# Kernel optimization log

Hardware: AMD Instinct MI355X
Metric: run time of the kernel (lower is better)

## Reference

```python
import jax, jax.numpy as jnp
import numpy as np

B, DIM, H, W = 2, 256, 64, 64
HEADS, DIM_HEAD = 8, 64
DIM_INNER = HEADS * DIM_HEAD  # 512


def setup_inputs() -> dict:
    key = jax.random.key(0)
    k1, k2, k3 = jax.random.split(key, 3)
    fmap = jax.random.normal(k1, (B, DIM, H, W), dtype=jnp.float32)
    # 1x1 convs == channel matmuls; store as [out_ch, in_ch]
    w_qkv = jax.random.normal(k2, (3 * DIM_INNER, DIM), dtype=jnp.float32) * (DIM ** -0.5)
    w_out = jax.random.normal(k3, (DIM, DIM_INNER), dtype=jnp.float32) * (DIM_INNER ** -0.5)
    return {"fmap": fmap, "w_qkv": w_qkv, "w_out": w_out}


def reference(fmap, w_qkv, w_out):
    b, c, x, y = fmap.shape
    n = x * y
    h, d = HEADS, DIM_HEAD
    xt = fmap.reshape(b, c, n)                       # [B, C, N]
    qkv = jnp.einsum('oc,bcn->bon', w_qkv, xt)        # [B, 3*h*d, N]
    q, k, v = jnp.split(qkv, 3, axis=1)               # each [B, h*d, N]
    # -> [B, h, N, d]
    to_bhnd = lambda t: t.reshape(b, h, d, n).transpose(0, 1, 3, 2)
    q, k, v = to_bhnd(q), to_bhnd(k), to_bhnd(v)
    # Euclidean distance matrix (torch.cdist p=2)
    q2 = jnp.sum(q * q, axis=-1)                      # [B, h, N]
    k2 = jnp.sum(k * k, axis=-1)                      # [B, h, N]
    qk = jnp.einsum('bhid,bhjd->bhij', q, k)          # [B, h, N, N]
    sim = jnp.sqrt(jnp.maximum(q2[..., :, None] + k2[..., None, :] - 2.0 * qk, 0.0))
    attn = jax.nn.softmax(sim, axis=-1)
    out = jnp.einsum('bhij,bhjd->bhid', attn, v)      # [B, h, N, d]
    out = out.transpose(0, 1, 3, 2).reshape(b, h * d, n)  # [B, h*d, N]
    out = jnp.einsum('oc,bcn->bon', w_out, out)       # [B, dim, N]
    return out.reshape(b, c, x, y)
```

## Files before the change

kernel.cpp:

```cpp
#include <hip/hip_runtime.h>

#define B_      2
#define DIM_    256
#define N_      4096
#define HEADS_  8
#define DINNER_ 512

typedef _Float16 half_t;
typedef _Float16 half8  __attribute__((ext_vector_type(8)));
typedef _Float16 half4v __attribute__((ext_vector_type(4)));
typedef _Float16 half2v __attribute__((ext_vector_type(2)));
typedef float    floatx4 __attribute__((ext_vector_type(4)));

#define SCL_    1.4426950408889634f
#define SHIFT2_ 20.0f


__global__ __launch_bounds__(256) void prep_all(const float* __restrict__ fmap,
                                                const float* __restrict__ w_qkv,
                                                const float* __restrict__ w_out,
                                                half_t* __restrict__ wqF,
                                                half_t* __restrict__ woF,
                                                half_t* __restrict__ xTg) {
    const int t = threadIdx.x, bx = blockIdx.x;
    __shared__ float Tl[64 * 68];
    if (bx < 96) {
        half_t* dst = wqF + (size_t)bx * 4096;
#pragma unroll
        for (int j = 0; j < 2; ++j) {
            const int cch = j * 256 + t;
            const int o = cch >> 4, m15 = cch & 15;
            const float4 a  = *(const float4*)&w_qkv[(size_t)(bx * 16 + m15) * 256 + o * 8];
            const float4 bb = *(const float4*)&w_qkv[(size_t)(bx * 16 + m15) * 256 + o * 8 + 4];
            half8 hv;
            hv[0] = (half_t)a.x;  hv[1] = (half_t)a.y;  hv[2] = (half_t)a.z;  hv[3] = (half_t)a.w;
            hv[4] = (half_t)bb.x; hv[5] = (half_t)bb.y; hv[6] = (half_t)bb.z; hv[7] = (half_t)bb.w;
            *(half8*)(dst + o * 128 + m15 * 8) = hv;
        }
    } else if (bx < 112) {
        const int mt = bx - 96;
        half_t* dst = woF + (size_t)mt * 8192;
#pragma unroll
        for (int j = 0; j < 4; ++j) {
            const int cch = j * 256 + t;
            const int o = cch >> 4, m15 = cch & 15;
            const float4 a  = *(const float4*)&w_out[(size_t)(mt * 16 + m15) * 512 + o * 8];
            const float4 bb = *(const float4*)&w_out[(size_t)(mt * 16 + m15) * 512 + o * 8 + 4];
            half8 hv;
            hv[0] = (half_t)a.x;  hv[1] = (half_t)a.y;  hv[2] = (half_t)a.z;  hv[3] = (half_t)a.w;
            hv[4] = (half_t)bb.x; hv[5] = (half_t)bb.y; hv[6] = (half_t)bb.z; hv[7] = (half_t)bb.w;
            *(half8*)(dst + o * 128 + m15 * 8) = hv;
        }
    } else {
        const int idx = bx - 112;
        const int n0 = (idx & 63) * 64, k0 = ((idx >> 6) & 3) * 64, b = idx >> 8;
        {
            const int kk = t >> 2, nq = (t & 3) * 16;
#pragma unroll
            for (int q = 0; q < 4; ++q) {
                float4 v = *(const float4*)&fmap[((size_t)b * DIM_ + k0 + kk) * N_ + n0 + nq + 4 * q];
                *(float4*)&Tl[kk * 68 + nq + 4 * q] = v;
            }
        }
        __syncthreads();
        {
            const int n = t >> 2, ko = (t & 3) * 16;
            half8 h0, h1;
#pragma unroll
            for (int j = 0; j < 8; ++j) h0[j] = (half_t)Tl[(ko + j) * 68 + n];
#pragma unroll
            for (int j = 0; j < 8; ++j) h1[j] = (half_t)Tl[(ko + 8 + j) * 68 + n];
            half_t* dst = xTg + (((size_t)b * 64 + (n0 >> 6)) * 4 + (k0 >> 6)) * 4096;
            const int o0 = ((ko >> 5) * 4 + (n >> 4)) * 512 + (((ko >> 3) & 3) * 16 + (n & 15)) * 8;
            const int k8 = ko + 8;
            const int o1 = ((k8 >> 5) * 4 + (n >> 4)) * 512 + (((k8 >> 3) & 3) * 16 + (n & 15)) * 8;
            *(half8*)(dst + o0) = h0;
            *(half8*)(dst + o1) = h1;
        }
    }
}

__global__ __launch_bounds__(256) void mm_qkv_mf(const half_t* __restrict__ wqF,
                                                 const half_t* __restrict__ xTg,
                                                 half_t* __restrict__ perm,
                                                 float* __restrict__ sq) {
    const int nt64 = blockIdx.x, by = blockIdx.y, b = blockIdx.z;
    const int t = threadIdx.x, w = t >> 6, L = t & 63, c = L & 15, g = L >> 4;
    const int mt = by * 4 + w;

    const half_t* Ab = wqF + (size_t)mt * 4096;
    const half_t* Bb = xTg + (((size_t)b * 64 + nt64) * 4) * 4096;

    __shared__ __align__(16) char smraw[8192 + 4352];
    half_t* VtH = (half_t*)smraw;
    float*  red = (float*)(smraw + 8192);

    const floatx4 fz = {0.f, 0.f, 0.f, 0.f};
    floatx4 acc[4];
#pragma unroll
    for (int ns = 0; ns < 4; ++ns) acc[ns] = fz;

#pragma unroll
    for (int kc = 0; kc < 8; ++kc) {
        const half8 af = *(const half8*)(Ab + (kc * 4 + g) * 128 + c * 8);
        const half_t* Bs = Bb + (kc >> 1) * 4096 + (kc & 1) * 2048;
#pragma unroll
        for (int ns = 0; ns < 4; ++ns) {
            const half8 bf = *(const half8*)(Bs + ns * 512 + L * 8);
            acc[ns] = __builtin_amdgcn_mfma_f32_16x16x32_f16(af, bf, acc[ns], 0, 0, 0);
        }
    }

    half_t* dst = perm + (((size_t)(b * 24 + by) * 64 + nt64) << 12);
    if (by < 16) {
        float part[4];
#pragma unroll
        for (int ns = 0; ns < 4; ++ns) {
            half_t hv[4];
            float s = 0.f;
#pragma unroll
            for (int i = 0; i < 4; ++i) {
                hv[i] = (half_t)(acc[ns][i] * SCL_);
                const float f = (float)hv[i];
                s = fmaf(f, f, s);
            }
            part[ns] = s;
            const int off = ((w >> 1) * 4 + ns) * 512 + (((2 * w + (g >> 1)) & 3) * 16 + c) * 8 + 4 * (g & 1);
            half2v p0, p1;
            p0[0] = hv[0]; p0[1] = hv[1];
            p1[0] = hv[2]; p1[1] = hv[3];
            *(half2v*)(VtH + off)     = p0;
            *(half2v*)(VtH + off + 2) = p1;
        }
#pragma unroll
        for (int ns = 0; ns < 4; ++ns)
            red[(ns * 16 + (w * 4 + g)) * 17 + c] = part[ns];
        __syncthreads();
#pragma unroll
        for (int j = 0; j < 2; ++j)
            *(half8*)(dst + t * 16 + j * 8) = *(half8*)(VtH + t * 16 + j * 8);
        if (t < 64) {
            const int ns = t >> 4, cc = t & 15;
            float s = 0.f;
#pragma unroll
            for (int wg = 0; wg < 16; ++wg) s += red[(ns * 16 + wg) * 17 + cc];
            const int tens = by >> 3, hh = by & 7;
            sq[((size_t)(tens * 16 + b * 8 + hh)) * N_ + nt64 * 64 + ns * 16 + cc] = s;
        }
    } else {
#pragma unroll
        for (int ns = 0; ns < 4; ++ns)
#pragma unroll
            for (int i = 0; i < 4; ++i)
                VtH[((ns >> 1) * 4 + w) * 512 + ((c >> 2) * 16 + 4 * g + i) * 8 + (ns & 1) * 4 + (c & 3)] =
                    (half_t)acc[ns][i];
        __syncthreads();
#pragma unroll
        for (int j = 0; j < 2; ++j)
            *(half8*)(dst + t * 16 + j * 8) = *(half8*)(VtH + t * 16 + j * 8);
    }
}

__global__ __launch_bounds__(512) void attn_mfma(const half_t* __restrict__ perm,
                                                 const float* __restrict__ sq,
                                                 half_t* __restrict__ oh,
                                                 float* __restrict__ lbuf) {
    const int bx = blockIdx.x;
    const int qb = bx & 15, kh = bx >> 4;
    const int h = blockIdx.y, b = blockIdx.z;
    const int bh = b * HEADS_ + h;

    const half_t* Qb = perm + ((size_t)(b * 24 + h) << 18);
    const half_t* Kb = perm + ((size_t)(b * 24 + 8 + h) << 18);
    const half_t* Vb = perm + ((size_t)(b * 24 + 16 + h) << 18);
    const float* q2a = sq + (size_t)bh * N_;
    const float* k2a = sq + (size_t)(16 + bh) * N_;

    __shared__ __align__(16) half_t Kl[2][4096];
    __shared__ __align__(16) half_t Vl[2][4096];
    __shared__ __align__(16) float  k2l[1024];

    const int t = threadIdx.x, w = t >> 6, L = t & 63, c = L & 15, g = L >> 4;
    const floatx4 fz = {0.f, 0.f, 0.f, 0.f};

    *(float2*)&k2l[t * 2] = *(const float2*)&k2a[kh * 1024 + t * 2];

    const int tl = w >> 1;
    const int p0 = (w & 1) * 2, p1 = p0 + 1;
    const half_t* Qt = Qb + ((size_t)(qb * 4 + tl) << 12);
    const half8 bq0a = *(const half8*)(Qt + (0 * 4 + p0) * 512 + L * 8);
    const half8 bq1a = *(const half8*)(Qt + (1 * 4 + p0) * 512 + L * 8);
    const half8 bq0b = *(const half8*)(Qt + (0 * 4 + p1) * 512 + L * 8);
    const half8 bq1b = *(const half8*)(Qt + (1 * 4 + p1) * 512 + L * 8);
    const float q2la = q2a[qb * 256 + 64 * tl + 16 * p0 + c];
    const float q2lb = q2a[qb * 256 + 64 * tl + 16 * p1 + c];

    half8 aone8;
    {
        const half_t ov = (c == 0) ? (half_t)1.0f : (half_t)0.0f;
        aone8[0] = ov; aone8[1] = ov; aone8[2] = ov; aone8[3] = ov;
        aone8[4] = ov; aone8[5] = ov; aone8[6] = ov; aone8[7] = ov;
    }

    floatx4 Oa[4], Ob[4];
    floatx4 laca = fz, lacb = fz;
#pragma unroll
    for (int dt = 0; dt < 4; ++dt) { Oa[dt] = fz; Ob[dt] = fz; }

    const int kt0 = kh * 16;
    half8 rk = *(const half8*)(Kb + ((size_t)kt0 << 12) + t * 8);
    half8 rv = *(const half8*)(Vb + ((size_t)kt0 << 12) + t * 8);

    union H8 { half8 v; half2v h2[4]; };

    for (int it = 0; it < 16; ++it) {
        const int buf = it & 1;
        *(half8*)(&Kl[buf][t * 8]) = rk;
        *(half8*)(&Vl[buf][t * 8]) = rv;
        asm volatile("s_waitcnt lgkmcnt(0)\n\ts_barrier" ::: "memory");
        if (it < 15) {
            rk = *(const half8*)(Kb + ((size_t)(kt0 + it + 1) << 12) + t * 8);
            rv = *(const half8*)(Vb + ((size_t)(kt0 + it + 1) << 12) + t * 8);
        }

#pragma unroll
        for (int ntp = 0; ntp < 2; ++ntp) {
            H8 ua, ub;
#pragma unroll
            for (int hh = 0; hh < 2; ++hh) {
                const int nt = ntp * 2 + hh;
                const half8 ak0 = *(const half8*)(&Kl[buf][(0 * 4 + nt) * 512 + L * 8]);
                const half8 ak1 = *(const half8*)(&Kl[buf][(1 * 4 + nt) * 512 + L * 8]);
                floatx4 Sa = __builtin_amdgcn_mfma_f32_16x16x32_f16(ak0, bq0a, fz, 0, 0, 0);
                Sa = __builtin_amdgcn_mfma_f32_16x16x32_f16(ak1, bq1a, Sa, 0, 0, 0);
                floatx4 Sb = __builtin_amdgcn_mfma_f32_16x16x32_f16(ak0, bq0b, fz, 0, 0, 0);
                Sb = __builtin_amdgcn_mfma_f32_16x16x32_f16(ak1, bq1b, Sb, 0, 0, 0);
                const float4 k2v = *(const float4*)&k2l[it * 64 + 16 * nt + 4 * g];

                float pa[4], pb[4];
                const float k2arr[4] = {k2v.x, k2v.y, k2v.z, k2v.w};
#pragma unroll
                for (int i = 0; i < 4; ++i) {
                    pa[i] = __builtin_amdgcn_exp2f(
                        __builtin_amdgcn_sqrtf(__builtin_fabsf(fmaf(Sa[i], -2.0f, q2la + k2arr[i]))) - SHIFT2_);
                    pb[i] = __builtin_amdgcn_exp2f(
                        __builtin_amdgcn_sqrtf(__builtin_fabsf(fmaf(Sb[i], -2.0f, q2lb + k2arr[i]))) - SHIFT2_);
                }
                ua.h2[2 * hh]     = __builtin_bit_cast(half2v, __builtin_amdgcn_cvt_pkrtz(pa[0], pa[1]));
                ua.h2[2 * hh + 1] = __builtin_bit_cast(half2v, __builtin_amdgcn_cvt_pkrtz(pa[2], pa[3]));
                ub.h2[2 * hh]     = __builtin_bit_cast(half2v, __builtin_amdgcn_cvt_pkrtz(pb[0], pb[1]));
                ub.h2[2 * hh + 1] = __builtin_bit_cast(half2v, __builtin_amdgcn_cvt_pkrtz(pb[2], pb[3]));
            }

            laca = __builtin_amdgcn_mfma_f32_16x16x32_f16(aone8, ua.v, laca, 0, 0, 0);
            lacb = __builtin_amdgcn_mfma_f32_16x16x32_f16(aone8, ub.v, lacb, 0, 0, 0);
#pragma unroll
            for (int dt = 0; dt < 4; ++dt) {
                const half8 av = *(const half8*)(&Vl[buf][(ntp * 4 + dt) * 512 + L * 8]);
                Oa[dt] = __builtin_amdgcn_mfma_f32_16x16x32_f16(av, ua.v, Oa[dt], 0, 0, 0);
                Ob[dt] = __builtin_amdgcn_mfma_f32_16x16x32_f16(av, ub.v, Ob[dt], 0, 0, 0);
            }
        }
    }

    const int ntile = qb * 4 + tl;
    half_t* dst = oh + (size_t)kh * 4194304 + (((size_t)bh * 64 + ntile) << 12);
#pragma unroll
    for (int dt = 0; dt < 4; ++dt) {
        const int obase = ((dt >> 1) * 4) * 512 + (((2 * dt + (g >> 1)) & 3) * 16 + c) * 8 + 4 * (g & 1);
        const half2v a0 = __builtin_bit_cast(half2v, __builtin_amdgcn_cvt_pkrtz(Oa[dt][0], Oa[dt][1]));
        const half2v a1 = __builtin_bit_cast(half2v, __builtin_amdgcn_cvt_pkrtz(Oa[dt][2], Oa[dt][3]));
        *(half2v*)(dst + obase + p0 * 512)     = a0;
        *(half2v*)(dst + obase + p0 * 512 + 2) = a1;
        const half2v b0 = __builtin_bit_cast(half2v, __builtin_amdgcn_cvt_pkrtz(Ob[dt][0], Ob[dt][1]));
        const half2v b1 = __builtin_bit_cast(half2v, __builtin_amdgcn_cvt_pkrtz(Ob[dt][2], Ob[dt][3]));
        *(half2v*)(dst + obase + p1 * 512)     = b0;
        *(half2v*)(dst + obase + p1 * 512 + 2) = b1;
    }
    if (L < 16) {
        const size_t lb0 = (size_t)kh * 65536 + (size_t)bh * N_ + qb * 256 + 64 * tl;
        lbuf[lb0 + 16 * p0 + L] = laca[0];
        lbuf[lb0 + 16 * p1 + L] = lacb[0];
    }
}

__global__ __launch_bounds__(256) void mm_out_mf(const half_t* __restrict__ woF,
                                                 const half_t* __restrict__ oh,
                                                 const float* __restrict__ lbuf,
                                                 float* __restrict__ out) {
    const int nt64 = blockIdx.x, mb = blockIdx.y, b = blockIdx.z;
    const int t = threadIdx.x, w = t >> 6, L = t & 63, c = L & 15, g = L >> 4;
    const int mt = mb * 4 + w;

    const half_t* Ab = woF + (size_t)mt * 8192;
    const floatx4 fz = {0.f, 0.f, 0.f, 0.f};
    floatx4 O4[4];
#pragma unroll
    for (int ns = 0; ns < 4; ++ns) O4[ns] = fz;

    __shared__ __align__(16) half_t sh[2][4096];
    __shared__ float lsh[2][64];

    half8 r0[4], r1[4];
    float lr[4];

    auto LOADH = [&](int h) {
        const size_t toff = (((size_t)(b * 8 + h) * 64 + nt64) << 12) + t * 16;
#pragma unroll
        for (int q = 0; q < 4; ++q) {
            r0[q] = *(const half8*)(oh + (size_t)q * 4194304 + toff);
            r1[q] = *(const half8*)(oh + (size_t)q * 4194304 + toff + 8);
        }
        if (t < 64) {
            const size_t li = (size_t)(b * 8 + h) * N_ + nt64 * 64 + t;
#pragma unroll
            for (int q = 0; q < 4; ++q) lr[q] = lbuf[(size_t)q * 65536 + li];
        }
    };

    LOADH(0);
    for (int h = 0; h < 8; ++h) {
        const int buf = h & 1;
        const half8 s0 = (r0[0] + r0[1]) + (r0[2] + r0[3]);
        const half8 s1 = (r1[0] + r1[1]) + (r1[2] + r1[3]);
        *(half8*)(&sh[buf][t * 16])     = s0;
        *(half8*)(&sh[buf][t * 16 + 8]) = s1;
        if (t < 64)
            lsh[buf][t] = __builtin_amdgcn_rcpf((lr[0] + lr[1]) + (lr[2] + lr[3]));
        __syncthreads();
        if (h < 7) LOADH(h + 1);

        floatx4 acc[4];
#pragma unroll
        for (int ns = 0; ns < 4; ++ns) acc[ns] = fz;
#pragma unroll
        for (int c2 = 0; c2 < 2; ++c2) {
            const half8 af = *(const half8*)(Ab + (h * 8 + c2 * 4 + g) * 128 + c * 8);
#pragma unroll
            for (int ns = 0; ns < 4; ++ns) {
                const half8 bf = *(const half8*)(&sh[buf][(c2 * 4 + ns) * 512 + L * 8]);
                acc[ns] = __builtin_amdgcn_mfma_f32_16x16x32_f16(af, bf, acc[ns], 0, 0, 0);
            }
        }
#pragma unroll
        for (int ns = 0; ns < 4; ++ns) {
            const float inv = lsh[buf][ns * 16 + c];
#pragma unroll
            for (int i = 0; i < 4; ++i) O4[ns][i] = fmaf(acc[ns][i], inv, O4[ns][i]);
        }
    }

    float* Cg = out + ((size_t)b * DIM_ + mt * 16) * N_ + nt64 * 64;
#pragma unroll
    for (int ns = 0; ns < 4; ++ns)
#pragma unroll
        for (int i = 0; i < 4; ++i)
            Cg[(size_t)(4 * g + i) * N_ + ns * 16 + c] = O4[ns][i];
}

extern "C" void kernel_launch(void* const* d_in, const int* in_sizes, int n_in,
                              void* d_out, int out_size, void* d_ws, size_t ws_size,
                              hipStream_t stream) {
    const float* fmap  = (const float*)d_in[0];
    const float* w_qkv = (const float*)d_in[1];
    const float* w_out = (const float*)d_in[2];
    float* out = (float*)d_out;

    char* ws = (char*)d_ws;
    half_t* perm = (half_t*)ws;
    float*  sq   = (float*) (ws + 25165824);
    float*  lbuf = (float*) (ws + 25690112);
    half_t* woF  = (half_t*)(ws + 26738688);
    half_t* oh   = (half_t*)(ws + 27000832);
    half_t* xTg  = (half_t*)(ws + 27000832);
    half_t* wqF  = (half_t*)(ws + 31195136);

    prep_all <<<624, 256, 0, stream>>>(fmap, w_qkv, w_out, wqF, woF, xTg);
    mm_qkv_mf<<<dim3(64, 24, 2), 256, 0, stream>>>(wqF, xTg, perm, sq);
    attn_mfma<<<dim3(64, 8, 2), 512, 0, stream>>>(perm, sq, oh, lbuf);
    mm_out_mf<<<dim3(64, 4, 2), 256, 0, stream>>>(woF, oh, lbuf, out);
}
```

Measured before the change: 191.0 us.

## Use direct global-to-LDS loads in attention, smaller blocks, and LDS-staged QKV B tiles

The attention kernel now runs 256-thread blocks over 128 query rows each, doubling the grid and raising occupancy (launch bounds 256, 8). It replaces register-staged double-buffered K/V tiles with single-buffered global_load_lds transfers that go straight into shared memory. This drops register pressure and LDS footprint but exposes load latency, since each tile now waits on vmcnt(0) with no prefetch overlap. The QKV projection also stages its B operand through shared memory in two phases instead of reading it directly from global memory.

```diff
diff --git a/kernel.cpp b/kernel.cpp
--- a/kernel.cpp
+++ b/kernel.cpp
@@ -15,6 +15,11 @@
 #define SCL_    1.4426950408889634f
 #define SHIFT2_ 20.0f
 
+
+__device__ __forceinline__ void gll16(const void* g, void* l) {
+    __builtin_amdgcn_global_load_lds((const __attribute__((address_space(1))) void*)g,
+                                     (__attribute__((address_space(3))) void*)l, 16, 0, 0);
+}
 
 __global__ __launch_bounds__(256) void prep_all(const float* __restrict__ fmap,
                                                 const float* __restrict__ w_qkv,
@@ -91,7 +96,8 @@
     const half_t* Ab = wqF + (size_t)mt * 4096;
     const half_t* Bb = xTg + (((size_t)b * 64 + nt64) * 4) * 4096;
 
-    __shared__ __align__(16) char smraw[8192 + 4352];
+    __shared__ __align__(16) char smraw[16384];
+    half_t* Bsh = (half_t*)smraw;
     half_t* VtH = (half_t*)smraw;
     float*  red = (float*)(smraw + 8192);
 
@@ -101,15 +107,25 @@
     for (int ns = 0; ns < 4; ++ns) acc[ns] = fz;
 
 #pragma unroll
-    for (int kc = 0; kc < 8; ++kc) {
-        const half8 af = *(const half8*)(Ab + (kc * 4 + g) * 128 + c * 8);
-        const half_t* Bs = Bb + (kc >> 1) * 4096 + (kc & 1) * 2048;
-#pragma unroll
-        for (int ns = 0; ns < 4; ++ns) {
-            const half8 bf = *(const half8*)(Bs + ns * 512 + L * 8);
-            acc[ns] = __builtin_amdgcn_mfma_f32_16x16x32_f16(af, bf, acc[ns], 0, 0, 0);
-        }
-    }
+    for (int ph = 0; ph < 2; ++ph) {
+        if (ph) __syncthreads();
+#pragma unroll
+        for (int j = 0; j < 4; ++j)
+            *(half8*)&Bsh[(j * 256 + t) * 8] = *(const half8*)(Bb + ph * 8192 + (j * 256 + t) * 8);
+        __syncthreads();
+#pragma unroll
+        for (int kk = 0; kk < 4; ++kk) {
+            const int kc = ph * 4 + kk;
+            const half8 af = *(const half8*)(Ab + (kc * 4 + g) * 128 + c * 8);
+            const half_t* Bs = Bsh + (kk >> 1) * 4096 + (kk & 1) * 2048;
+#pragma unroll
+            for (int ns = 0; ns < 4; ++ns) {
+                const half8 bf = *(const half8*)(Bs + ns * 512 + L * 8);
+                acc[ns] = __builtin_amdgcn_mfma_f32_16x16x32_f16(af, bf, acc[ns], 0, 0, 0);
+            }
+        }
+    }
+    __syncthreads();
 
     half_t* dst = perm + (((size_t)(b * 24 + by) * 64 + nt64) << 12);
     if (by < 16) {
@@ -161,12 +177,12 @@
     }
 }
 
-__global__ __launch_bounds__(512) void attn_mfma(const half_t* __restrict__ perm,
-                                                 const float* __restrict__ sq,
-                                                 half_t* __restrict__ oh,
-                                                 float* __restrict__ lbuf) {
+__global__ __launch_bounds__(256, 8) void attn_mfma(const half_t* __restrict__ perm,
+                                                    const float* __restrict__ sq,
+                                                    half_t* __restrict__ oh,
+                                                    float* __restrict__ lbuf) {
     const int bx = blockIdx.x;
-    const int qb = bx & 15, kh = bx >> 4;
+    const int qb = bx & 31, kh = bx >> 5;
     const int h = blockIdx.y, b = blockIdx.z;
     const int bh = b * HEADS_ + h;
 
@@ -176,24 +192,24 @@
     const float* q2a = sq + (size_t)bh * N_;
     const float* k2a = sq + (size_t)(16 + bh) * N_;
 
-    __shared__ __align__(16) half_t Kl[2][4096];
-    __shared__ __align__(16) half_t Vl[2][4096];
+    __shared__ __align__(16) half_t Kl[4096];
+    __shared__ __align__(16) half_t Vl[4096];
     __shared__ __align__(16) float  k2l[1024];
 
     const int t = threadIdx.x, w = t >> 6, L = t & 63, c = L & 15, g = L >> 4;
     const floatx4 fz = {0.f, 0.f, 0.f, 0.f};
 
-    *(float2*)&k2l[t * 2] = *(const float2*)&k2a[kh * 1024 + t * 2];
+    *(float4*)&k2l[t * 4] = *(const float4*)&k2a[kh * 1024 + t * 4];
 
     const int tl = w >> 1;
     const int p0 = (w & 1) * 2, p1 = p0 + 1;
-    const half_t* Qt = Qb + ((size_t)(qb * 4 + tl) << 12);
+    const half_t* Qt = Qb + ((size_t)(qb * 2 + tl) << 12);
     const half8 bq0a = *(const half8*)(Qt + (0 * 4 + p0) * 512 + L * 8);
     const half8 bq1a = *(const half8*)(Qt + (1 * 4 + p0) * 512 + L * 8);
     const half8 bq0b = *(const half8*)(Qt + (0 * 4 + p1) * 512 + L * 8);
     const half8 bq1b = *(const half8*)(Qt + (1 * 4 + p1) * 512 + L * 8);
-    const float q2la = q2a[qb * 256 + 64 * tl + 16 * p0 + c];
-    const float q2lb = q2a[qb * 256 + 64 * tl + 16 * p1 + c];
+    const float q2la = q2a[qb * 128 + 64 * tl + 16 * p0 + c];
+    const float q2lb = q2a[qb * 128 + 64 * tl + 16 * p1 + c];
 
     half8 aone8;
     {
@@ -208,20 +224,20 @@
     for (int dt = 0; dt < 4; ++dt) { Oa[dt] = fz; Ob[dt] = fz; }
 
     const int kt0 = kh * 16;
-    half8 rk = *(const half8*)(Kb + ((size_t)kt0 << 12) + t * 8);
-    half8 rv = *(const half8*)(Vb + ((size_t)kt0 << 12) + t * 8);
-
     union H8 { half8 v; half2v h2[4]; };
 
     for (int it = 0; it < 16; ++it) {
-        const int buf = it & 1;
-        *(half8*)(&Kl[buf][t * 8]) = rk;
-        *(half8*)(&Vl[buf][t * 8]) = rv;
-        asm volatile("s_waitcnt lgkmcnt(0)\n\ts_barrier" ::: "memory");
-        if (it < 15) {
-            rk = *(const half8*)(Kb + ((size_t)(kt0 + it + 1) << 12) + t * 8);
-            rv = *(const half8*)(Vb + ((size_t)(kt0 + it + 1) << 12) + t * 8);
-        }
+        asm volatile("s_barrier" ::: "memory");
+        {
+            const half_t* gK = Kb + ((size_t)(kt0 + it) << 12);
+            const half_t* gV = Vb + ((size_t)(kt0 + it) << 12);
+#pragma unroll
+            for (int j = 0; j < 2; ++j) {
+                gll16(gK + j * 2048 + t * 8, &Kl[j * 2048 + w * 512]);
+                gll16(gV + j * 2048 + t * 8, &Vl[j * 2048 + w * 512]);
+            }
+        }
+        asm volatile("s_waitcnt vmcnt(0) lgkmcnt(0)\n\ts_barrier" ::: "memory");
 
 #pragma unroll
         for (int ntp = 0; ntp < 2; ++ntp) {
@@ -229,8 +245,8 @@
 #pragma unroll
             for (int hh = 0; hh < 2; ++hh) {
                 const int nt = ntp * 2 + hh;
-                const half8 ak0 = *(const half8*)(&Kl[buf][(0 * 4 + nt) * 512 + L * 8]);
-                const half8 ak1 = *(const half8*)(&Kl[buf][(1 * 4 + nt) * 512 + L * 8]);
+                const half8 ak0 = *(const half8*)(&Kl[(0 * 4 + nt) * 512 + L * 8]);
+                const half8 ak1 = *(const half8*)(&Kl[(1 * 4 + nt) * 512 + L * 8]);
                 floatx4 Sa = __builtin_amdgcn_mfma_f32_16x16x32_f16(ak0, bq0a, fz, 0, 0, 0);
                 Sa = __builtin_amdgcn_mfma_f32_16x16x32_f16(ak1, bq1a, Sa, 0, 0, 0);
                 floatx4 Sb = __builtin_amdgcn_mfma_f32_16x16x32_f16(ak0, bq0b, fz, 0, 0, 0);
@@ -256,14 +272,14 @@
             lacb = __builtin_amdgcn_mfma_f32_16x16x32_f16(aone8, ub.v, lacb, 0, 0, 0);
 #pragma unroll
             for (int dt = 0; dt < 4; ++dt) {
-                const half8 av = *(const half8*)(&Vl[buf][(ntp * 4 + dt) * 512 + L * 8]);
+                const half8 av = *(const half8*)(&Vl[(ntp * 4 + dt) * 512 + L * 8]);
                 Oa[dt] = __builtin_amdgcn_mfma_f32_16x16x32_f16(av, ua.v, Oa[dt], 0, 0, 0);
                 Ob[dt] = __builtin_amdgcn_mfma_f32_16x16x32_f16(av, ub.v, Ob[dt], 0, 0, 0);
             }
         }
     }
 
-    const int ntile = qb * 4 + tl;
+    const int ntile = qb * 2 + tl;
     half_t* dst = oh + (size_t)kh * 4194304 + (((size_t)bh * 64 + ntile) << 12);
 #pragma unroll
     for (int dt = 0; dt < 4; ++dt) {
@@ -278,7 +294,7 @@
         *(half2v*)(dst + obase + p1 * 512 + 2) = b1;
     }
     if (L < 16) {
-        const size_t lb0 = (size_t)kh * 65536 + (size_t)bh * N_ + qb * 256 + 64 * tl;
+        const size_t lb0 = (size_t)kh * 65536 + (size_t)bh * N_ + qb * 128 + 64 * tl;
         lbuf[lb0 + 16 * p0 + L] = laca[0];
         lbuf[lb0 + 16 * p1 + L] = lacb[0];
     }
@@ -377,6 +393,6 @@
 
     prep_all <<<624, 256, 0, stream>>>(fmap, w_qkv, w_out, wqF, woF, xTg);
     mm_qkv_mf<<<dim3(64, 24, 2), 256, 0, stream>>>(wqF, xTg, perm, sq);
-    attn_mfma<<<dim3(64, 8, 2), 512, 0, stream>>>(perm, sq, oh, lbuf);
+    attn_mfma<<<dim3(128, 8, 2), 256, 0, stream>>>(perm, sq, oh, lbuf);
     mm_out_mf<<<dim3(64, 4, 2), 256, 0, stream>>>(woF, oh, lbuf, out);
 }
```

Result: slower. 754.9 us (+295.2%).

## Fold squared norms into extra MFMA and stage QKV B tiles in LDS

Applied to the files above, without the earlier changes.

The attention kernel now folds the q² and k² norm terms and the -2 scale into the score MFMA. Q is stored pre-scaled by -2, and one extra MFMA per tile multiplies a padded k² (as a split hi/lo fp16 pair) by ones plus ones by q². This removes the per-element FMA and the float4 LDS read of k² from the exp loop. The QKV projection also stages the B operand through LDS in two phases instead of reading it straight from global memory. The cost is an extra MFMA per score tile, a small precision loss from splitting the norms into fp16 hi/lo parts, and more barriers in the projection kernel.

```diff
diff --git a/kernel.cpp b/kernel.cpp
--- a/kernel.cpp
+++ b/kernel.cpp
@@ -91,7 +91,8 @@
     const half_t* Ab = wqF + (size_t)mt * 4096;
     const half_t* Bb = xTg + (((size_t)b * 64 + nt64) * 4) * 4096;
 
-    __shared__ __align__(16) char smraw[8192 + 4352];
+    __shared__ __align__(16) char smraw[16384];
+    half_t* Bsh = (half_t*)smraw;
     half_t* VtH = (half_t*)smraw;
     float*  red = (float*)(smraw + 8192);
 
@@ -101,36 +102,48 @@
     for (int ns = 0; ns < 4; ++ns) acc[ns] = fz;
 
 #pragma unroll
-    for (int kc = 0; kc < 8; ++kc) {
-        const half8 af = *(const half8*)(Ab + (kc * 4 + g) * 128 + c * 8);
-        const half_t* Bs = Bb + (kc >> 1) * 4096 + (kc & 1) * 2048;
-#pragma unroll
-        for (int ns = 0; ns < 4; ++ns) {
-            const half8 bf = *(const half8*)(Bs + ns * 512 + L * 8);
-            acc[ns] = __builtin_amdgcn_mfma_f32_16x16x32_f16(af, bf, acc[ns], 0, 0, 0);
-        }
-    }
+    for (int ph = 0; ph < 2; ++ph) {
+        if (ph) __syncthreads();
+#pragma unroll
+        for (int j = 0; j < 4; ++j)
+            *(half8*)&Bsh[(j * 256 + t) * 8] = *(const half8*)(Bb + ph * 8192 + (j * 256 + t) * 8);
+        __syncthreads();
+#pragma unroll
+        for (int kk = 0; kk < 4; ++kk) {
+            const int kc = ph * 4 + kk;
+            const half8 af = *(const half8*)(Ab + (kc * 4 + g) * 128 + c * 8);
+            const half_t* Bs = Bsh + (kk >> 1) * 4096 + (kk & 1) * 2048;
+#pragma unroll
+            for (int ns = 0; ns < 4; ++ns) {
+                const half8 bf = *(const half8*)(Bs + ns * 512 + L * 8);
+                acc[ns] = __builtin_amdgcn_mfma_f32_16x16x32_f16(af, bf, acc[ns], 0, 0, 0);
+            }
+        }
+    }
+    __syncthreads();
 
     half_t* dst = perm + (((size_t)(b * 24 + by) * 64 + nt64) << 12);
     if (by < 16) {
+        const float qs = (by < 8) ? -2.0f : 1.0f;
         float part[4];
 #pragma unroll
         for (int ns = 0; ns < 4; ++ns) {
-            half_t hv[4];
+            half_t m[4];
             float s = 0.f;
 #pragma unroll
             for (int i = 0; i < 4; ++i) {
-                hv[i] = (half_t)(acc[ns][i] * SCL_);
-                const float f = (float)hv[i];
+                const half_t hq = (half_t)(acc[ns][i] * SCL_);
+                const float f = (float)hq;
                 s = fmaf(f, f, s);
+                m[i] = (half_t)(qs * f);
             }
             part[ns] = s;
             const int off = ((w >> 1) * 4 + ns) * 512 + (((2 * w + (g >> 1)) & 3) * 16 + c) * 8 + 4 * (g & 1);
-            half2v p0, p1;
-            p0[0] = hv[0]; p0[1] = hv[1];
-            p1[0] = hv[2]; p1[1] = hv[3];
-            *(half2v*)(VtH + off)     = p0;
-            *(half2v*)(VtH + off + 2) = p1;
+            half2v p0v, p1v;
+            p0v[0] = m[0]; p0v[1] = m[1];
+            p1v[0] = m[2]; p1v[1] = m[3];
+            *(half2v*)(VtH + off)     = p0v;
+            *(half2v*)(VtH + off + 2) = p1v;
         }
 #pragma unroll
         for (int ns = 0; ns < 4; ++ns)
@@ -178,12 +191,20 @@
 
     __shared__ __align__(16) half_t Kl[2][4096];
     __shared__ __align__(16) half_t Vl[2][4096];
-    __shared__ __align__(16) float  k2l[1024];
+    __shared__ __align__(16) unsigned int k2lp[1024];
 
     const int t = threadIdx.x, w = t >> 6, L = t & 63, c = L & 15, g = L >> 4;
     const floatx4 fz = {0.f, 0.f, 0.f, 0.f};
 
-    *(float2*)&k2l[t * 2] = *(const float2*)&k2a[kh * 1024 + t * 2];
+    {
+        const float2 kv = *(const float2*)&k2a[kh * 1024 + t * 2];
+        const half_t h0 = (half_t)kv.x; const half_t l0 = (half_t)(kv.x - (float)h0);
+        const half_t h1 = (half_t)kv.y; const half_t l1 = (half_t)(kv.y - (float)h1);
+        k2lp[t * 2]     = (unsigned)__builtin_bit_cast(unsigned short, h0) |
+                          ((unsigned)__builtin_bit_cast(unsigned short, l0) << 16);
+        k2lp[t * 2 + 1] = (unsigned)__builtin_bit_cast(unsigned short, h1) |
+                          ((unsigned)__builtin_bit_cast(unsigned short, l1) << 16);
+    }
 
     const int tl = w >> 1;
     const int p0 = (w & 1) * 2, p1 = p0 + 1;
@@ -192,8 +213,24 @@
     const half8 bq1a = *(const half8*)(Qt + (1 * 4 + p0) * 512 + L * 8);
     const half8 bq0b = *(const half8*)(Qt + (0 * 4 + p1) * 512 + L * 8);
     const half8 bq1b = *(const half8*)(Qt + (1 * 4 + p1) * 512 + L * 8);
-    const float q2la = q2a[qb * 256 + 64 * tl + 16 * p0 + c];
-    const float q2lb = q2a[qb * 256 + 64 * tl + 16 * p1 + c];
+
+    union U8 { half8 v; unsigned int u[4]; };
+    U8 qXa, qXb;
+    {
+        const float q2la = q2a[qb * 256 + 64 * tl + 16 * p0 + c];
+        const float q2lb = q2a[qb * 256 + 64 * tl + 16 * p1 + c];
+        const half_t ha = (half_t)q2la; const half_t la = (half_t)(q2la - (float)ha);
+        const half_t hb = (half_t)q2lb; const half_t lb_ = (half_t)(q2lb - (float)hb);
+        const unsigned pka = (unsigned)__builtin_bit_cast(unsigned short, ha) |
+                             ((unsigned)__builtin_bit_cast(unsigned short, la) << 16);
+        const unsigned pkb = (unsigned)__builtin_bit_cast(unsigned short, hb) |
+                             ((unsigned)__builtin_bit_cast(unsigned short, lb_) << 16);
+        const bool lo16 = (L < 16);
+        qXa.u[0] = lo16 ? pka : 0u; qXa.u[1] = lo16 ? 0x3C003C00u : 0u;
+        qXa.u[2] = 0u; qXa.u[3] = 0u;
+        qXb.u[0] = lo16 ? pkb : 0u; qXb.u[1] = lo16 ? 0x3C003C00u : 0u;
+        qXb.u[2] = 0u; qXb.u[3] = 0u;
+    }
 
     half8 aone8;
     {
@@ -231,20 +268,24 @@
                 const int nt = ntp * 2 + hh;
                 const half8 ak0 = *(const half8*)(&Kl[buf][(0 * 4 + nt) * 512 + L * 8]);
                 const half8 ak1 = *(const half8*)(&Kl[buf][(1 * 4 + nt) * 512 + L * 8]);
+                U8 kX;
+                kX.u[0] = 0x3C003C00u;
+                kX.u[1] = k2lp[it * 64 + nt * 16 + c];
+                kX.u[2] = 0u; kX.u[3] = 0u;
                 floatx4 Sa = __builtin_amdgcn_mfma_f32_16x16x32_f16(ak0, bq0a, fz, 0, 0, 0);
                 Sa = __builtin_amdgcn_mfma_f32_16x16x32_f16(ak1, bq1a, Sa, 0, 0, 0);
+                Sa = __builtin_amdgcn_mfma_f32_16x16x32_f16(kX.v, qXa.v, Sa, 0, 0, 0);
                 floatx4 Sb = __builtin_amdgcn_mfma_f32_16x16x32_f16(ak0, bq0b, fz, 0, 0, 0);
                 Sb = __builtin_amdgcn_mfma_f32_16x16x32_f16(ak1, bq1b, Sb, 0, 0, 0);
-                const float4 k2v = *(const float4*)&k2l[it * 64 + 16 * nt + 4 * g];
+                Sb = __builtin_amdgcn_mfma_f32_16x16x32_f16(kX.v, qXb.v, Sb, 0, 0, 0);
 
                 float pa[4], pb[4];
-                const float k2arr[4] = {k2v.x, k2v.y, k2v.z, k2v.w};
 #pragma unroll
                 for (int i = 0; i < 4; ++i) {
                     pa[i] = __builtin_amdgcn_exp2f(
-                        __builtin_amdgcn_sqrtf(__builtin_fabsf(fmaf(Sa[i], -2.0f, q2la + k2arr[i]))) - SHIFT2_);
+                        __builtin_amdgcn_sqrtf(__builtin_fabsf(Sa[i])) - SHIFT2_);
                     pb[i] = __builtin_amdgcn_exp2f(
-                        __builtin_amdgcn_sqrtf(__builtin_fabsf(fmaf(Sb[i], -2.0f, q2lb + k2arr[i]))) - SHIFT2_);
+                        __builtin_amdgcn_sqrtf(__builtin_fabsf(Sb[i])) - SHIFT2_);
                 }
                 ua.h2[2 * hh]     = __builtin_bit_cast(half2v, __builtin_amdgcn_cvt_pkrtz(pa[0], pa[1]));
                 ua.h2[2 * hh + 1] = __builtin_bit_cast(half2v, __builtin_amdgcn_cvt_pkrtz(pa[2], pa[3]));
```

Measured after the change: 181.7 us. 4.9% less time.
